# Performance work log

Measured on AMD Instinct MI355X. Metric: run time of the kernel, lower is better.

Reference implementation:

```python
import jax, jax.numpy as jnp
import numpy as np

BN_EPS = 1e-5


def _knn_idx(pos, k):
    # pos: (B, 3, N). Nearest-k by squared euclidean distance (self included).
    sq = jnp.sum(pos * pos, axis=1)                        # (B, N)
    inner = jnp.einsum('bcn,bcm->bnm', pos, pos)           # (B, N, N)
    neg_dist = 2.0 * inner - sq[:, :, None] - sq[:, None, :]
    _, idx = jax.lax.top_k(neg_dist, k)                    # (B, N, k)
    return idx


def setup_inputs() -> dict:
    key = jax.random.key(0)
    k1, k2, k3 = jax.random.split(key, 3)
    B, C, N, K, D = 4, 64, 8192, 16, 64
    return {
        'x': jax.random.normal(k1, (B, C, N), dtype=jnp.float32),
        'pos': jax.random.normal(k2, (B, 3, N), dtype=jnp.float32),
        'spectral_filter': jax.random.normal(k3, (K, C, D), dtype=jnp.float32),
        'gamma': jnp.ones((D,), dtype=jnp.float32),
        'beta': jnp.zeros((D,), dtype=jnp.float32),
    }


def reference(x, pos, spectral_filter, gamma, beta):
    k = spectral_filter.shape[0]
    idx = _knn_idx(pos, k)                                  # (B, N, k) int32
    # gather neighbors: nb[b, c, n, j] = x[b, c, idx[b, n, j]]
    nb = jax.vmap(lambda xf, ii: xf[:, ii])(x, idx)         # (B, C, N, k)
    edge = nb - x[:, :, :, None]                            # (B, C, N, k)
    # per-k small GEMM: 'bnkc,kcd->bnd' (channel dim is axis 1 here)
    out = jnp.einsum('bcnk,kcd->bnd', edge, spectral_filter)
    out = out.transpose(0, 2, 1)                            # (B, D, N)
    # BatchNorm1d, training mode (biased variance over batch and points)
    mean = jnp.mean(out, axis=(0, 2), keepdims=True)
    var = jnp.var(out, axis=(0, 2), keepdims=True)
    out = (out - mean) * jax.lax.rsqrt(var + BN_EPS)
    return out * gamma[None, :, None] + beta[None, :, None]
```

## Files before the change

### kernel.cpp

```cpp
#include <hip/hip_runtime.h>
#include <hip/hip_bf16.h>

#define NPTS 8192
#define NQ   32768
#define KNN  16
#define SCAP 112

#define OFF_XT   0
#define OFF_FBIG (8*1024*1024)
#define OFF_SUMS (OFF_FBIG + 278528)
#define OFF_IDX  (OFF_SUMS + 512)
#define OFF_PRE  (OFF_IDX + 2*1024*1024)

__device__ __forceinline__ float sq3(float x, float y, float z) {
    #pragma clang fp contract(off)
    float xx = x * x;
    float yy = y * y;
    float zz = z * z;
    return (xx + yy) + zz;
}
__device__ __forceinline__ float negd2(float qx, float qy, float qz, float sqn,
                                       float mx, float my, float mz, float sqm) {
    #pragma clang fp contract(off)
    float p0 = qx * mx;
    float inn = __builtin_fmaf(qz, mz, __builtin_fmaf(qy, my, p0));
    float t = 2.0f * inn;
    float u = t - sqn;
    return u - sqm;
}
#define KEY_EPS2 2.0e-3f

__global__ __launch_bounds__(256) void k_prep(const float* __restrict__ x,
                                              const float* __restrict__ F,
                                              float* __restrict__ xT,
                                              float* __restrict__ Fb,
                                              float* __restrict__ sums) {
    int bid = blockIdx.x;
    if (bid < 512) {
        __shared__ float tile[64][65];
        int lane = threadIdx.x & 63, wid = threadIdx.x >> 6;
        int b = bid >> 7, nt = bid & 127;
        int n0 = nt * 64;
        for (int rr = 0; rr < 16; ++rr) {
            int c = wid * 16 + rr;
            tile[c][lane] = x[((size_t)b * 64 + c) * NPTS + n0 + lane];
        }
        __syncthreads();
        for (int rr = 0; rr < 16; ++rr) {
            int r = wid * 16 + rr;
            xT[((size_t)(b * NPTS + n0 + r)) * 64 + lane] = tile[lane][r];
        }
    } else if (bid < 528) {
        int j = bid - 512;
        for (int e = threadIdx.x; e < 4096; e += 256)
            Fb[j * 4096 + e] = F[j * 4096 + e];
    } else if (bid == 528) {
        for (int e = threadIdx.x; e < 4096; e += 256) {
            float s = 0.f;
            for (int k = 0; k < 16; ++k) s += F[k * 4096 + e];
            Fb[16 * 4096 + e] = -s;
        }
    } else {
        if (threadIdx.x < 128) sums[threadIdx.x] = 0.f;
    }
}

#define TILE 1024
__global__ __launch_bounds__(256) void k_knn(const float* __restrict__ pos,
                                             int* __restrict__ idxo) {
    __shared__ float Xs[TILE], Ys[TILE], Zs[TILE], Ss[TILE];
    __shared__ int            cnt[32];
    __shared__ unsigned short sidx[32][SCAP];
    __shared__ float          skey[32][SCAP];
    __shared__ int            outI[32][16];
    int t = threadIdx.x, lane = t & 63, wid = t >> 6;
    int qblk = blockIdx.x * 32;
    int b = qblk >> 13;
    const float* px = pos + (size_t)b * 3 * NPTS;
    const float* py = px + NPTS;
    const float* pz = py + NPTS;
    int n0 = (qblk & (NPTS - 1)) + wid * 8;

    float qxs[8], qys[8], qzs[8], sqs[8], tqx[8], tqy[8], tqz[8];
    #pragma unroll
    for (int i = 0; i < 8; ++i) {
        qxs[i] = px[n0 + i]; qys[i] = py[n0 + i]; qzs[i] = pz[n0 + i];
        sqs[i] = sq3(qxs[i], qys[i], qzs[i]);
        tqx[i] = 2.0f * qxs[i]; tqy[i] = 2.0f * qys[i]; tqz[i] = 2.0f * qzs[i];
    }
    if (lane < 8) cnt[wid * 8 + lane] = 0;
    if (lane < 16) {
        #pragma unroll
        for (int i = 0; i < 8; ++i) outI[wid * 8 + i][lane] = n0 + i;
    }

    float lm[8];
    #pragma unroll
    for (int i = 0; i < 8; ++i) lm[i] = -3.4e38f;

    for (int tile = 0; tile < 8; ++tile) {
        int tb = tile * TILE;
        {
            float4 xv = *(const float4*)(px + tb + t * 4);
            float4 yv = *(const float4*)(py + tb + t * 4);
            float4 zv = *(const float4*)(pz + tb + t * 4);
            float4 sv;
            sv.x = sq3(xv.x, yv.x, zv.x); sv.y = sq3(xv.y, yv.y, zv.y);
            sv.z = sq3(xv.z, yv.z, zv.z); sv.w = sq3(xv.w, yv.w, zv.w);
            *(float4*)&Xs[t * 4] = xv; *(float4*)&Ys[t * 4] = yv;
            *(float4*)&Zs[t * 4] = zv; *(float4*)&Ss[t * 4] = sv;
        }
        __syncthreads();
        #pragma unroll
        for (int it = 0; it < 4; ++it) {
            int ml = it * 256 + lane * 4;
            float4 X = *(const float4*)&Xs[ml];
            float4 Y = *(const float4*)&Ys[ml];
            float4 Z = *(const float4*)&Zs[ml];
            float4 S = *(const float4*)&Ss[ml];
            #pragma unroll
            for (int i = 0; i < 8; ++i) {
                float a0 = __builtin_fmaf(tqx[i], X.x, __builtin_fmaf(tqy[i], Y.x, __builtin_fmaf(tqz[i], Z.x, -S.x)));
                float a1 = __builtin_fmaf(tqx[i], X.y, __builtin_fmaf(tqy[i], Y.y, __builtin_fmaf(tqz[i], Z.y, -S.y)));
                float a2 = __builtin_fmaf(tqx[i], X.z, __builtin_fmaf(tqy[i], Y.z, __builtin_fmaf(tqz[i], Z.z, -S.z)));
                float a3 = __builtin_fmaf(tqx[i], X.w, __builtin_fmaf(tqy[i], Y.w, __builtin_fmaf(tqz[i], Z.w, -S.w)));
                lm[i] = fmaxf(lm[i], fmaxf(fmaxf(a0, a1), fmaxf(a2, a3)));
            }
        }
        __syncthreads();
    }

    float thr[8];
    #pragma unroll
    for (int i = 0; i < 8; ++i) {
        float val = lm[i], tv = 0.f;
        for (int r = 0; r < 16; ++r) {
            float mm = val;
            mm = fmaxf(mm, __shfl_xor(mm, 1, 64));
            mm = fmaxf(mm, __shfl_xor(mm, 2, 64));
            mm = fmaxf(mm, __shfl_xor(mm, 4, 64));
            mm = fmaxf(mm, __shfl_xor(mm, 8, 64));
            mm = fmaxf(mm, __shfl_xor(mm, 16, 64));
            mm = fmaxf(mm, __shfl_xor(mm, 32, 64));
            tv = mm;
            if (val == mm) val = -3.4e38f;
        }
        thr[i] = tv - KEY_EPS2;
    }

    for (int tile = 0; tile < 8; ++tile) {
        int tb = tile * TILE;
        {
            float4 xv = *(const float4*)(px + tb + t * 4);
            float4 yv = *(const float4*)(py + tb + t * 4);
            float4 zv = *(const float4*)(pz + tb + t * 4);
            float4 sv;
            sv.x = sq3(xv.x, yv.x, zv.x); sv.y = sq3(xv.y, yv.y, zv.y);
            sv.z = sq3(xv.z, yv.z, zv.z); sv.w = sq3(xv.w, yv.w, zv.w);
            *(float4*)&Xs[t * 4] = xv; *(float4*)&Ys[t * 4] = yv;
            *(float4*)&Zs[t * 4] = zv; *(float4*)&Ss[t * 4] = sv;
        }
        __syncthreads();
        #pragma unroll
        for (int it = 0; it < 4; ++it) {
            int ml = it * 256 + lane * 4;
            int m = tb + ml;
            float4 X = *(const float4*)&Xs[ml];
            float4 Y = *(const float4*)&Ys[ml];
            float4 Z = *(const float4*)&Zs[ml];
            float4 S = *(const float4*)&Ss[ml];
            #pragma unroll
            for (int i = 0; i < 8; ++i) {
                int lq = wid * 8 + i;
                float a0 = __builtin_fmaf(tqx[i], X.x, __builtin_fmaf(tqy[i], Y.x, __builtin_fmaf(tqz[i], Z.x, -S.x)));
                float a1 = __builtin_fmaf(tqx[i], X.y, __builtin_fmaf(tqy[i], Y.y, __builtin_fmaf(tqz[i], Z.y, -S.y)));
                float a2 = __builtin_fmaf(tqx[i], X.z, __builtin_fmaf(tqy[i], Y.z, __builtin_fmaf(tqz[i], Z.z, -S.z)));
                float a3 = __builtin_fmaf(tqx[i], X.w, __builtin_fmaf(tqy[i], Y.w, __builtin_fmaf(tqz[i], Z.w, -S.w)));
                if (a0 >= thr[i]) { int s_ = atomicAdd(&cnt[lq],1); if (s_<SCAP) sidx[lq][s_] = (unsigned short)m; }
                if (a1 >= thr[i]) { int s_ = atomicAdd(&cnt[lq],1); if (s_<SCAP) sidx[lq][s_] = (unsigned short)(m+1); }
                if (a2 >= thr[i]) { int s_ = atomicAdd(&cnt[lq],1); if (s_<SCAP) sidx[lq][s_] = (unsigned short)(m+2); }
                if (a3 >= thr[i]) { int s_ = atomicAdd(&cnt[lq],1); if (s_<SCAP) sidx[lq][s_] = (unsigned short)(m+3); }
            }
        }
        __syncthreads();
    }

    #pragma unroll 1
    for (int i = 0; i < 8; ++i) {
        int lq = wid * 8 + i;
        int S = cnt[lq]; if (S > SCAP) S = SCAP;
        for (int p = lane; p < S; p += 64) {
            int m = sidx[lq][p];
            float mx = px[m], my = py[m], mz = pz[m];
            skey[lq][p] = negd2(qxs[i], qys[i], qzs[i], sqs[i],
                                mx, my, mz, sq3(mx, my, mz));
        }
    }

    #pragma unroll 1
    for (int i = 0; i < 8; ++i) {
        int lq = wid * 8 + i;
        int S = cnt[lq]; if (S > SCAP) S = SCAP;
        for (int p = lane; p < S; p += 64) {
            int m = sidx[lq][p];
            float km = skey[lq][p];
            int rank = 0;
            for (int j = 0; j < S; ++j) {
                float kj = skey[lq][j];
                int ij = sidx[lq][j];
                if (kj > km || (kj == km && ij < m)) rank++;
            }
            if (rank < KNN) outI[lq][rank] = m;
        }
    }
    __syncthreads();
    #pragma unroll
    for (int h = 0; h < 2; ++h) {
        int lq = h * 16 + (t >> 4);
        idxo[(size_t)(qblk + lq) * KNN + (t & 15)] = outI[lq][t & 15];
    }
}

#define CPAD 68
__global__ __launch_bounds__(256) void k_conv(const float* __restrict__ xT,
                                              const float* __restrict__ Fb,
                                              const int* __restrict__ idx,
                                              float* __restrict__ outp,
                                              float* __restrict__ sums) {
    __shared__ float At[64][CPAD];
    __shared__ float Bt[64 * 64];
    int t = threadIdx.x;
    int q0 = blockIdx.x * 64;
    int bbase = q0 & ~(NPTS - 1);
    int qi0 = (t >> 4) * 4;
    int dj0 = (t & 15) * 4;
    int r = t & 63;
    int s = t >> 6;

    float acc[4][4];
    #pragma unroll
    for (int a = 0; a < 4; ++a)
        #pragma unroll
        for (int bb = 0; bb < 4; ++bb) acc[a][bb] = 0.f;

    for (int j = 0; j < 17; ++j) {
        {
            int qg = q0 + r;
            int nbr = (j < 16) ? (idx[(size_t)qg * KNN + j] & (NPTS - 1))
                               : (qg & (NPTS - 1));
            const float* src = xT + ((size_t)(bbase + nbr) * 64 + s * 16);
            float4 v0 = *(const float4*)(src);
            float4 v1 = *(const float4*)(src + 4);
            float4 v2 = *(const float4*)(src + 8);
            float4 v3 = *(const float4*)(src + 12);
            int c0 = s * 16;
            At[c0+ 0][r] = v0.x; At[c0+ 1][r] = v0.y; At[c0+ 2][r] = v0.z; At[c0+ 3][r] = v0.w;
            At[c0+ 4][r] = v1.x; At[c0+ 5][r] = v1.y; At[c0+ 6][r] = v1.z; At[c0+ 7][r] = v1.w;
            At[c0+ 8][r] = v2.x; At[c0+ 9][r] = v2.y; At[c0+10][r] = v2.z; At[c0+11][r] = v2.w;
            At[c0+12][r] = v3.x; At[c0+13][r] = v3.y; At[c0+14][r] = v3.z; At[c0+15][r] = v3.w;
        }
        {
            const float* fj = Fb + j * 4096;
            #pragma unroll
            for (int u = 0; u < 4; ++u) {
                int e = u * 1024 + t * 4;
                *(float4*)&Bt[e] = *(const float4*)(fj + e);
            }
        }
        __syncthreads();
        #pragma unroll 8
        for (int k = 0; k < 64; ++k) {
            float4 av = *(const float4*)&At[k][qi0];
            float4 bv = *(const float4*)&Bt[k * 64 + dj0];
            acc[0][0] = fmaf(av.x, bv.x, acc[0][0]);
            acc[0][1] = fmaf(av.x, bv.y, acc[0][1]);
            acc[0][2] = fmaf(av.x, bv.z, acc[0][2]);
            acc[0][3] = fmaf(av.x, bv.w, acc[0][3]);
            acc[1][0] = fmaf(av.y, bv.x, acc[1][0]);
            acc[1][1] = fmaf(av.y, bv.y, acc[1][1]);
            acc[1][2] = fmaf(av.y, bv.z, acc[1][2]);
            acc[1][3] = fmaf(av.y, bv.w, acc[1][3]);
            acc[2][0] = fmaf(av.z, bv.x, acc[2][0]);
            acc[2][1] = fmaf(av.z, bv.y, acc[2][1]);
            acc[2][2] = fmaf(av.z, bv.z, acc[2][2]);
            acc[2][3] = fmaf(av.z, bv.w, acc[2][3]);
            acc[3][0] = fmaf(av.w, bv.x, acc[3][0]);
            acc[3][1] = fmaf(av.w, bv.y, acc[3][1]);
            acc[3][2] = fmaf(av.w, bv.z, acc[3][2]);
            acc[3][3] = fmaf(av.w, bv.w, acc[3][3]);
        }
        __syncthreads();
    }
    #pragma unroll
    for (int qi = 0; qi < 4; ++qi) {
        float4 o = make_float4(acc[qi][0], acc[qi][1], acc[qi][2], acc[qi][3]);
        *(float4*)(outp + (size_t)(q0 + qi0 + qi) * 64 + dj0) = o;
    }
    {
        float* P  = Bt;
        float* P2 = Bt + 1024;
        int g = t >> 4;
        #pragma unroll
        for (int dd = 0; dd < 4; ++dd) {
            float sv = ((acc[0][dd] + acc[1][dd]) + acc[2][dd]) + acc[3][dd];
            float qv = fmaf(acc[3][dd], acc[3][dd],
                       fmaf(acc[2][dd], acc[2][dd],
                       fmaf(acc[1][dd], acc[1][dd], acc[0][dd] * acc[0][dd])));
            P [g * 64 + dj0 + dd] = sv;
            P2[g * 64 + dj0 + dd] = qv;
        }
        __syncthreads();
        if (t < 64) {
            float a = 0.f, b2 = 0.f;
            #pragma unroll
            for (int gg = 0; gg < 16; ++gg) {
                a  += P [gg * 64 + t];
                b2 += P2[gg * 64 + t];
            }
            atomicAdd(&sums[t], a);
            atomicAdd(&sums[64 + t], b2);
        }
    }
}

__global__ __launch_bounds__(256) void k_bn(const float* __restrict__ outp,
                                            const float* __restrict__ sums,
                                            const float* __restrict__ gamma,
                                            const float* __restrict__ beta,
                                            float* __restrict__ out) {
    __shared__ float tile[64][65];
    __shared__ float sa[64], sb[64];
    int lane = threadIdx.x & 63, wid = threadIdx.x >> 6;
    int b = blockIdx.x >> 7, nt = blockIdx.x & 127;
    int n0 = nt * 64;
    if (threadIdx.x < 64) {
        const float inv = 1.f / 32768.f;
        float mean = sums[threadIdx.x] * inv;
        float var = sums[64 + threadIdx.x] * inv - mean * mean;
        float rs = rsqrtf(var + 1e-5f);
        float a = rs * gamma[threadIdx.x];
        sa[threadIdx.x] = a;
        sb[threadIdx.x] = beta[threadIdx.x] - mean * a;
    }
    for (int rr = 0; rr < 16; ++rr) {
        int r = wid * 16 + rr;
        tile[r][lane] = outp[((size_t)(b * NPTS + n0 + r)) * 64 + lane];
    }
    __syncthreads();
    for (int rr = 0; rr < 16; ++rr) {
        int dr = wid * 16 + rr;
        out[((size_t)b * 64 + dr) * NPTS + n0 + lane] =
            fmaf(tile[lane][dr], sa[dr], sb[dr]);
    }
}

extern "C" void kernel_launch(void* const* d_in, const int* in_sizes, int n_in,
                              void* d_out, int out_size, void* d_ws, size_t ws_size,
                              hipStream_t stream) {
    (void)in_sizes; (void)n_in; (void)out_size; (void)ws_size;
    const float* x     = (const float*)d_in[0];
    const float* pos   = (const float*)d_in[1];
    const float* F     = (const float*)d_in[2];
    const float* gamma = (const float*)d_in[3];
    const float* beta  = (const float*)d_in[4];
    float* out = (float*)d_out;

    char* ws = (char*)d_ws;
    float* xT   = (float*)(ws + OFF_XT);
    float* Fb   = (float*)(ws + OFF_FBIG);
    float* sums = (float*)(ws + OFF_SUMS);
    int*   idx  = (int*)(ws + OFF_IDX);
    float* pre  = (float*)(ws + OFF_PRE);

    k_prep<<<530, 256, 0, stream>>>(x, F, xT, Fb, sums);
    k_knn<<<1024, 256, 0, stream>>>(pos, idx);
    k_conv<<<512, 256, 0, stream>>>(xT, Fb, idx, pre, sums);
    k_bn<<<512, 256, 0, stream>>>(pre, sums, gamma, beta, out);
}
```

Measured before the change: 290.4 us.

## Precompute squared norms and stream kNN candidates from global memory without LDS tiles

Adds a pass in the prep kernel that computes per-point squared norms into a workspace slot reusing the pre buffer. The kNN kernel then reads coordinates and norms straight from global memory (L1/L2 cached) instead of staging 1024-point tiles in shared memory with barriers. It also sets a min-blocks-per-CU hint of 4. This removes per-tile recomputation, syncthreads and LDS usage, trading them for more global/cache load traffic per wave.

```diff
diff --git a/kernel.cpp b/kernel.cpp
--- a/kernel.cpp
+++ b/kernel.cpp
@@ -11,6 +11,7 @@
 #define OFF_SUMS (OFF_FBIG + 278528)
 #define OFF_IDX  (OFF_SUMS + 512)
 #define OFF_PRE  (OFF_IDX + 2*1024*1024)
+#define OFF_SQ   OFF_PRE
 
 __device__ __forceinline__ float sq3(float x, float y, float z) {
     #pragma clang fp contract(off)
@@ -32,9 +33,11 @@
 
 __global__ __launch_bounds__(256) void k_prep(const float* __restrict__ x,
                                               const float* __restrict__ F,
+                                              const float* __restrict__ pos,
                                               float* __restrict__ xT,
                                               float* __restrict__ Fb,
-                                              float* __restrict__ sums) {
+                                              float* __restrict__ sums,
+                                              float* __restrict__ sqa) {
     int bid = blockIdx.x;
     if (bid < 512) {
         __shared__ float tile[64][65];
@@ -60,15 +63,19 @@
             for (int k = 0; k < 16; ++k) s += F[k * 4096 + e];
             Fb[16 * 4096 + e] = -s;
         }
+    } else if (bid == 529) {
+        if (threadIdx.x < 128) sums[threadIdx.x] = 0.f;
     } else {
-        if (threadIdx.x < 128) sums[threadIdx.x] = 0.f;
-    }
-}
-
-#define TILE 1024
-__global__ __launch_bounds__(256) void k_knn(const float* __restrict__ pos,
-                                             int* __restrict__ idxo) {
-    __shared__ float Xs[TILE], Ys[TILE], Zs[TILE], Ss[TILE];
+        int g = (bid - 530) * 256 + threadIdx.x;
+        int b = g >> 13, n = g & (NPTS - 1);
+        const float* pb = pos + (size_t)b * 3 * NPTS;
+        sqa[g] = sq3(pb[n], pb[NPTS + n], pb[2 * NPTS + n]);
+    }
+}
+
+__global__ __launch_bounds__(256, 4) void k_knn(const float* __restrict__ pos,
+                                                const float* __restrict__ sqa,
+                                                int* __restrict__ idxo) {
     __shared__ int            cnt[32];
     __shared__ unsigned short sidx[32][SCAP];
     __shared__ float          skey[32][SCAP];
@@ -79,13 +86,14 @@
     const float* px = pos + (size_t)b * 3 * NPTS;
     const float* py = px + NPTS;
     const float* pz = py + NPTS;
+    const float* sb = sqa + (size_t)b * NPTS;
     int n0 = (qblk & (NPTS - 1)) + wid * 8;
 
     float qxs[8], qys[8], qzs[8], sqs[8], tqx[8], tqy[8], tqz[8];
     #pragma unroll
     for (int i = 0; i < 8; ++i) {
         qxs[i] = px[n0 + i]; qys[i] = py[n0 + i]; qzs[i] = pz[n0 + i];
-        sqs[i] = sq3(qxs[i], qys[i], qzs[i]);
+        sqs[i] = sb[n0 + i];
         tqx[i] = 2.0f * qxs[i]; tqy[i] = 2.0f * qys[i]; tqz[i] = 2.0f * qzs[i];
     }
     if (lane < 8) cnt[wid * 8 + lane] = 0;
@@ -97,37 +105,21 @@
     float lm[8];
     #pragma unroll
     for (int i = 0; i < 8; ++i) lm[i] = -3.4e38f;
-
-    for (int tile = 0; tile < 8; ++tile) {
-        int tb = tile * TILE;
-        {
-            float4 xv = *(const float4*)(px + tb + t * 4);
-            float4 yv = *(const float4*)(py + tb + t * 4);
-            float4 zv = *(const float4*)(pz + tb + t * 4);
-            float4 sv;
-            sv.x = sq3(xv.x, yv.x, zv.x); sv.y = sq3(xv.y, yv.y, zv.y);
-            sv.z = sq3(xv.z, yv.z, zv.z); sv.w = sq3(xv.w, yv.w, zv.w);
-            *(float4*)&Xs[t * 4] = xv; *(float4*)&Ys[t * 4] = yv;
-            *(float4*)&Zs[t * 4] = zv; *(float4*)&Ss[t * 4] = sv;
-        }
-        __syncthreads();
-        #pragma unroll
-        for (int it = 0; it < 4; ++it) {
-            int ml = it * 256 + lane * 4;
-            float4 X = *(const float4*)&Xs[ml];
-            float4 Y = *(const float4*)&Ys[ml];
-            float4 Z = *(const float4*)&Zs[ml];
-            float4 S = *(const float4*)&Ss[ml];
-            #pragma unroll
-            for (int i = 0; i < 8; ++i) {
-                float a0 = __builtin_fmaf(tqx[i], X.x, __builtin_fmaf(tqy[i], Y.x, __builtin_fmaf(tqz[i], Z.x, -S.x)));
-                float a1 = __builtin_fmaf(tqx[i], X.y, __builtin_fmaf(tqy[i], Y.y, __builtin_fmaf(tqz[i], Z.y, -S.y)));
-                float a2 = __builtin_fmaf(tqx[i], X.z, __builtin_fmaf(tqy[i], Y.z, __builtin_fmaf(tqz[i], Z.z, -S.z)));
-                float a3 = __builtin_fmaf(tqx[i], X.w, __builtin_fmaf(tqy[i], Y.w, __builtin_fmaf(tqz[i], Z.w, -S.w)));
-                lm[i] = fmaxf(lm[i], fmaxf(fmaxf(a0, a1), fmaxf(a2, a3)));
-            }
-        }
-        __syncthreads();
+    for (int it = 0; it < 32; ++it) {
+        int m = it * 256 + lane * 4;
+        float4 X = *(const float4*)(px + m);
+        float4 Y = *(const float4*)(py + m);
+        float4 Z = *(const float4*)(pz + m);
+        float4 S = *(const float4*)(sb + m);
+        #pragma unroll
+        for (int i = 0; i < 8; ++i) {
+            float a0 = __builtin_fmaf(tqx[i], X.x, __builtin_fmaf(tqy[i], Y.x, __builtin_fmaf(tqz[i], Z.x, -S.x)));
+            float a1 = __builtin_fmaf(tqx[i], X.y, __builtin_fmaf(tqy[i], Y.y, __builtin_fmaf(tqz[i], Z.y, -S.y)));
+            float a2 = __builtin_fmaf(tqx[i], X.z, __builtin_fmaf(tqy[i], Y.z, __builtin_fmaf(tqz[i], Z.z, -S.z)));
+            float a3 = __builtin_fmaf(tqx[i], X.w, __builtin_fmaf(tqy[i], Y.w, __builtin_fmaf(tqz[i], Z.w, -S.w)));
+            float m012 = fmaxf(fmaxf(a0, a1), a2);
+            lm[i] = fmaxf(fmaxf(m012, a3), lm[i]);
+        }
     }
 
     float thr[8];
@@ -148,41 +140,24 @@
         thr[i] = tv - KEY_EPS2;
     }
 
-    for (int tile = 0; tile < 8; ++tile) {
-        int tb = tile * TILE;
-        {
-            float4 xv = *(const float4*)(px + tb + t * 4);
-            float4 yv = *(const float4*)(py + tb + t * 4);
-            float4 zv = *(const float4*)(pz + tb + t * 4);
-            float4 sv;
-            sv.x = sq3(xv.x, yv.x, zv.x); sv.y = sq3(xv.y, yv.y, zv.y);
-            sv.z = sq3(xv.z, yv.z, zv.z); sv.w = sq3(xv.w, yv.w, zv.w);
-            *(float4*)&Xs[t * 4] = xv; *(float4*)&Ys[t * 4] = yv;
-            *(float4*)&Zs[t * 4] = zv; *(float4*)&Ss[t * 4] = sv;
-        }
-        __syncthreads();
-        #pragma unroll
-        for (int it = 0; it < 4; ++it) {
-            int ml = it * 256 + lane * 4;
-            int m = tb + ml;
-            float4 X = *(const float4*)&Xs[ml];
-            float4 Y = *(const float4*)&Ys[ml];
-            float4 Z = *(const float4*)&Zs[ml];
-            float4 S = *(const float4*)&Ss[ml];
-            #pragma unroll
-            for (int i = 0; i < 8; ++i) {
-                int lq = wid * 8 + i;
-                float a0 = __builtin_fmaf(tqx[i], X.x, __builtin_fmaf(tqy[i], Y.x, __builtin_fmaf(tqz[i], Z.x, -S.x)));
-                float a1 = __builtin_fmaf(tqx[i], X.y, __builtin_fmaf(tqy[i], Y.y, __builtin_fmaf(tqz[i], Z.y, -S.y)));
-                float a2 = __builtin_fmaf(tqx[i], X.z, __builtin_fmaf(tqy[i], Y.z, __builtin_fmaf(tqz[i], Z.z, -S.z)));
-                float a3 = __builtin_fmaf(tqx[i], X.w, __builtin_fmaf(tqy[i], Y.w, __builtin_fmaf(tqz[i], Z.w, -S.w)));
-                if (a0 >= thr[i]) { int s_ = atomicAdd(&cnt[lq],1); if (s_<SCAP) sidx[lq][s_] = (unsigned short)m; }
-                if (a1 >= thr[i]) { int s_ = atomicAdd(&cnt[lq],1); if (s_<SCAP) sidx[lq][s_] = (unsigned short)(m+1); }
-                if (a2 >= thr[i]) { int s_ = atomicAdd(&cnt[lq],1); if (s_<SCAP) sidx[lq][s_] = (unsigned short)(m+2); }
-                if (a3 >= thr[i]) { int s_ = atomicAdd(&cnt[lq],1); if (s_<SCAP) sidx[lq][s_] = (unsigned short)(m+3); }
-            }
-        }
-        __syncthreads();
+    for (int it = 0; it < 32; ++it) {
+        int m = it * 256 + lane * 4;
+        float4 X = *(const float4*)(px + m);
+        float4 Y = *(const float4*)(py + m);
+        float4 Z = *(const float4*)(pz + m);
+        float4 S = *(const float4*)(sb + m);
+        #pragma unroll
+        for (int i = 0; i < 8; ++i) {
+            int lq = wid * 8 + i;
+            float a0 = __builtin_fmaf(tqx[i], X.x, __builtin_fmaf(tqy[i], Y.x, __builtin_fmaf(tqz[i], Z.x, -S.x)));
+            float a1 = __builtin_fmaf(tqx[i], X.y, __builtin_fmaf(tqy[i], Y.y, __builtin_fmaf(tqz[i], Z.y, -S.y)));
+            float a2 = __builtin_fmaf(tqx[i], X.z, __builtin_fmaf(tqy[i], Y.z, __builtin_fmaf(tqz[i], Z.z, -S.z)));
+            float a3 = __builtin_fmaf(tqx[i], X.w, __builtin_fmaf(tqy[i], Y.w, __builtin_fmaf(tqz[i], Z.w, -S.w)));
+            if (a0 >= thr[i]) { int s_ = atomicAdd(&cnt[lq],1); if (s_<SCAP) sidx[lq][s_] = (unsigned short)m; }
+            if (a1 >= thr[i]) { int s_ = atomicAdd(&cnt[lq],1); if (s_<SCAP) sidx[lq][s_] = (unsigned short)(m+1); }
+            if (a2 >= thr[i]) { int s_ = atomicAdd(&cnt[lq],1); if (s_<SCAP) sidx[lq][s_] = (unsigned short)(m+2); }
+            if (a3 >= thr[i]) { int s_ = atomicAdd(&cnt[lq],1); if (s_<SCAP) sidx[lq][s_] = (unsigned short)(m+3); }
+        }
     }
 
     #pragma unroll 1
@@ -191,9 +166,8 @@
         int S = cnt[lq]; if (S > SCAP) S = SCAP;
         for (int p = lane; p < S; p += 64) {
             int m = sidx[lq][p];
-            float mx = px[m], my = py[m], mz = pz[m];
             skey[lq][p] = negd2(qxs[i], qys[i], qzs[i], sqs[i],
-                                mx, my, mz, sq3(mx, my, mz));
+                                px[m], py[m], pz[m], sb[m]);
         }
     }
 
@@ -371,9 +345,10 @@
     float* sums = (float*)(ws + OFF_SUMS);
     int*   idx  = (int*)(ws + OFF_IDX);
     float* pre  = (float*)(ws + OFF_PRE);
-
-    k_prep<<<530, 256, 0, stream>>>(x, F, xT, Fb, sums);
-    k_knn<<<1024, 256, 0, stream>>>(pos, idx);
+    float* sqa  = (float*)(ws + OFF_SQ);
+
+    k_prep<<<658, 256, 0, stream>>>(x, F, pos, xT, Fb, sums, sqa);
+    k_knn<<<1024, 256, 0, stream>>>(pos, sqa, idx);
     k_conv<<<512, 256, 0, stream>>>(xT, Fb, idx, pre, sums);
     k_bn<<<512, 256, 0, stream>>>(pre, sums, gamma, beta, out);
 }
```

Result: faster. 282.8 us (median of 3 runs) (-2.6%).
